# Kernel optimization log

Measured on AMD Instinct MI355X. Metric: run time of the kernel, lower is better.

Reference implementation:

```python
import jax, jax.numpy as jnp
import numpy as np


def setup_inputs() -> dict:
    key = jax.random.key(0)
    ks = jax.random.split(key, 7)
    B, I, H = 8192, 1024, 1024
    x = jax.random.normal(ks[0], (B, I), dtype=jnp.float32)
    h_prev = jax.random.normal(ks[1], (B, H), dtype=jnp.float32)
    C_prev = jax.random.normal(ks[2], (B, H), dtype=jnp.float32)
    W_f = jax.random.normal(ks[3], (I + H, H), dtype=jnp.float32) * 0.01
    W_i = jax.random.normal(ks[4], (I + H, H), dtype=jnp.float32) * 0.01
    W_C = jax.random.normal(ks[5], (I + H, H), dtype=jnp.float32) * 0.01
    W_o = jax.random.normal(ks[6], (I + H, H), dtype=jnp.float32) * 0.01
    b = jnp.zeros((H,), dtype=jnp.float32)
    return {"x": x, "h_prev": h_prev, "C_prev": C_prev,
            "W_f": W_f, "b_f": b, "W_i": W_i, "b_i": b,
            "W_C": W_C, "b_C": b, "W_o": W_o, "b_o": b}


def reference(x, h_prev, C_prev, W_f, b_f, W_i, b_i, W_C, b_C, W_o, b_o):
    combined = jnp.concatenate([x, h_prev], axis=1)  # [B, I+H]
    # Fuse the four gate GEMMs into one [B, I+H] x [I+H, 4H] matmul.
    W = jnp.concatenate([W_f, W_i, W_o, W_C], axis=1)  # [I+H, 4H]
    b = jnp.concatenate([b_f, b_i, b_o, b_C], axis=0)  # [4H]
    gates = combined @ W + b                            # [B, 4H]
    H = C_prev.shape[1]
    f_t = jax.nn.sigmoid(gates[:, 0:H])
    i_t = jax.nn.sigmoid(gates[:, H:2 * H])
    o_t = jax.nn.sigmoid(gates[:, 2 * H:3 * H])
    C_tilda = jnp.tanh(gates[:, 3 * H:4 * H])
    C_t = f_t * C_prev + i_t * C_tilda
    h_t = o_t * jnp.tanh(C_t)
    return (h_t, C_t)
```

## Files before the change

kernel.cpp:

```cpp
#include <hip/hip_runtime.h>
#include <hip/hip_bf16.h>

#define B_SZ 8192
#define IH   2048
#define H_SZ 1024
#define BM   256
#define BK   64
#define NT   (IH / BK)
#define NI   (NT / 2)
#define DBUF 65536
#define WOFF 32768

typedef __attribute__((ext_vector_type(8))) short  short8;
typedef __attribute__((ext_vector_type(4))) float  floatx4;

static __device__ __forceinline__ ushort f2bf(float f) {
  union { float f; unsigned u; } v; v.f = f;
  unsigned u = v.u;
  u += 0x7fffu + ((u >> 16) & 1u);
  return (ushort)(u >> 16);
}
static __device__ __forceinline__ float sigmoidf_(float x) {
  return 1.0f / (1.0f + __expf(-x));
}
static __device__ __forceinline__ float tanhf_(float x) {
  float ax = fabsf(x);
  float e = __expf(-2.0f * ax);
  float t = (1.0f - e) / (1.0f + e);
  return copysignf(t, x);
}
static __device__ __forceinline__ void gload_lds16(const void* gsrc, void* ldst) {
  __builtin_amdgcn_global_load_lds(
      (__attribute__((address_space(1))) const void*)gsrc,
      (__attribute__((address_space(3))) void*)ldst, 16, 0, 0);
}

__global__ __launch_bounds__(256) void convert_w_kernel(
    const float* __restrict__ Wf, const float* __restrict__ Wi,
    const float* __restrict__ Wo, const float* __restrict__ Wc,
    ushort* __restrict__ Wt) {
  __shared__ float tile[64][65];
  const int g  = blockIdx.z;
  const float* W = (g == 0) ? Wf : (g == 1) ? Wi : (g == 2) ? Wo : Wc;
  const int n0 = blockIdx.x * 64;
  const int k0 = blockIdx.y * 64;
  const int tid = threadIdx.x;
#pragma unroll
  for (int i = 0; i < 4; ++i) {
    int c = i * 256 + tid;
    int r = c >> 4, c4 = c & 15;
    float4 v = *(const float4*)(W + (size_t)(k0 + r) * H_SZ + n0 + c4 * 4);
    tile[r][c4 * 4 + 0] = v.x;
    tile[r][c4 * 4 + 1] = v.y;
    tile[r][c4 * 4 + 2] = v.z;
    tile[r][c4 * 4 + 3] = v.w;
  }
  __syncthreads();
  const int n  = tid >> 2;
  const int kc = (tid & 3) * 16;
  ushort o[16] __attribute__((aligned(16)));
#pragma unroll
  for (int e = 0; e < 16; ++e) o[e] = f2bf(tile[kc + e][n]);
  ushort* dst = Wt + ((size_t)g * H_SZ + n0 + n) * IH + k0 + kc;
  *(uint4*)(dst)     = *(uint4*)&o[0];
  *(uint4*)(dst + 8) = *(uint4*)&o[8];
}

__global__ __launch_bounds__(256) void convert_a_kernel(
    const float* __restrict__ x, const float* __restrict__ hp,
    ushort* __restrict__ Abf) {
  size_t idx = ((size_t)blockIdx.x * 256 + threadIdx.x) * 8;
  size_t row = idx >> 11;
  size_t col = idx & 2047;
  const float* src = (col < 1024) ? (x  + row * 1024 + col)
                                  : (hp + row * 1024 + (col - 1024));
  float4 v0 = *(const float4*)(src);
  float4 v1 = *(const float4*)(src + 4);
  ushort o[8] __attribute__((aligned(16)));
  o[0] = f2bf(v0.x); o[1] = f2bf(v0.y); o[2] = f2bf(v0.z); o[3] = f2bf(v0.w);
  o[4] = f2bf(v1.x); o[5] = f2bf(v1.y); o[6] = f2bf(v1.z); o[7] = f2bf(v1.w);
  *(uint4*)(Abf + idx) = *(uint4*)&o[0];
}

__global__ __launch_bounds__(512, 2) void lstm_fused_kernel(
    const float* __restrict__ Cp, const ushort* __restrict__ Wt,
    const ushort* __restrict__ Abf,
    const float* __restrict__ bf_, const float* __restrict__ bi_,
    const float* __restrict__ bo_, const float* __restrict__ bc_,
    float* __restrict__ out) {
  __shared__ char lds[2 * DBUF];

  const int bid = blockIdx.x;
  const int wg  = (bid & 7) * 64 + (bid >> 3);
  const int b0  = (wg >> 4) * BM;
  const int n0g = (wg & 15) * 64;

  const int tid = threadIdx.x;
  const int ln  = tid & 63;
  const int wv  = tid >> 6;
  const int wm  = wv >> 1, wn = wv & 1;

  floatx4 acc[4][8];
#pragma unroll
  for (int m = 0; m < 4; ++m)
#pragma unroll
    for (int j = 0; j < 8; ++j) acc[m][j] = {0.f, 0.f, 0.f, 0.f};

  const int sw  = (ln & 7) << 4;
  const int kb0 = (((ln >> 4) << 4)) ^ sw;
  const int kb1 = (64 + ((ln >> 4) << 4)) ^ sw;
  const int aR  = (wm * 64 + (ln & 15)) * 128;
  const int bR  = WOFF + (wn * 32 + (ln & 15)) * 128;
  int aB0[2], aB1[2], bB0[2], bB1[2];
#pragma unroll
  for (int d = 0; d < 2; ++d) {
    aB0[d] = d * DBUF + aR + kb0;  aB1[d] = d * DBUF + aR + kb1;
    bB0[d] = d * DBUF + bR + kb0;  bB1[d] = d * DBUF + bR + kb1;
  }

  const unsigned kcsw = ((tid & 7) * 16) ^ (((tid >> 3) & 7) << 4);
  const char*  AbfB = (const char*)Abf;
  const char*  WtB  = (const char*)Wt;
  unsigned aoff[2];
#pragma unroll
  for (int i = 0; i < 2; ++i)
    aoff[i] = ((unsigned)(b0 + i * 64 + (tid >> 3)) << 12) + kcsw;
  unsigned woff[2][2];
#pragma unroll
  for (int h = 0; h < 2; ++h)
#pragma unroll
    for (int i = 0; i < 2; ++i) {
      int nrt  = h * 128 + i * 64 + (tid >> 3);
      int g    = nrt >> 6, nloc = nrt & 63;
      woff[h][i] = ((unsigned)(g * H_SZ + n0g + nloc) << 12) + kcsw;
    }
  int dsto[2];
#pragma unroll
  for (int i = 0; i < 2; ++i) dsto[i] = (i * 512 + wv * 64) * 16;

#define STAGE_A(db, ktb, h)                                                   \
  do {                                                                        \
    gload_lds16(AbfB + (aoff[0] + ((unsigned)(h) << 19) + (unsigned)(ktb)),   \
                lds + (db) + (h) * 16384 + dsto[0]);                          \
    gload_lds16(AbfB + (aoff[1] + ((unsigned)(h) << 19) + (unsigned)(ktb)),   \
                lds + (db) + (h) * 16384 + dsto[1]);                          \
  } while (0)
#define STAGE_W(db, ktb, h)                                                   \
  do {                                                                        \
    gload_lds16(WtB + (woff[h][0] + (unsigned)(ktb)),                         \
                lds + (db) + WOFF + (h) * 16384 + dsto[0]);                   \
    gload_lds16(WtB + (woff[h][1] + (unsigned)(ktb)),                         \
                lds + (db) + WOFF + (h) * 16384 + dsto[1]);                   \
  } while (0)

  short8 aF[4][2];
  short8 bF[8][2];
#define RD_A(dbi, mf)                                                         \
  do {                                                                        \
    aF[mf][0] = *(const short8*)(lds + aB0[dbi] + (mf) * 2048);               \
    aF[mf][1] = *(const short8*)(lds + aB1[dbi] + (mf) * 2048);               \
  } while (0)
#define RD_B(dbi, j)                                                          \
  do {                                                                        \
    bF[j][0] = *(const short8*)(lds + bB0[dbi] + ((j) >> 1) * 8192 +          \
                                ((j) & 1) * 2048);                            \
    bF[j][1] = *(const short8*)(lds + bB1[dbi] + ((j) >> 1) * 8192 +          \
                                ((j) & 1) * 2048);                            \
  } while (0)
#define RDQA(d)  do { RD_A(d, 0); RD_A(d, 1); RD_A(d, 2); RD_A(d, 3); } while (0)
#define RDB03(d) do { RD_B(d, 0); RD_B(d, 1); RD_B(d, 2); RD_B(d, 3); } while (0)
#define RDB47(d) do { RD_B(d, 4); RD_B(d, 5); RD_B(d, 6); RD_B(d, 7); } while (0)
#define MFQ(jh)                                                               \
  do {                                                                        \
    __builtin_amdgcn_s_setprio(1);                                            \
    _Pragma("unroll")                                                         \
    for (int k_ = 0; k_ < 2; ++k_)                                            \
      _Pragma("unroll")                                                       \
      for (int mf_ = 0; mf_ < 4; ++mf_)                                       \
        _Pragma("unroll")                                                     \
        for (int j_ = 4 * (jh); j_ < 4 * (jh) + 4; ++j_)                      \
          acc[mf_][j_] = __builtin_amdgcn_mfma_f32_16x16x32_bf16(             \
              aF[mf_][k_], bF[j_][k_], acc[mf_][j_], 0, 0, 0);                \
    __builtin_amdgcn_s_setprio(0);                                            \
  } while (0)
#define BAR   __builtin_amdgcn_s_barrier()
#define VMC(n) asm volatile("s_waitcnt vmcnt(" #n ")" ::: "memory")

  STAGE_W(0, 0, 0); STAGE_A(0, 0, 0); STAGE_A(0, 0, 1); STAGE_W(0, 0, 1);
  STAGE_W(DBUF, 128, 0); STAGE_A(DBUF, 128, 0); STAGE_A(DBUF, 128, 1);
  VMC(6);
  BAR;

#pragma unroll 1
  for (int it = 0; it < NI; ++it) {
    const int kt1b  = (2 * it + 1) * 128;
    const int ktn0b = ((2 * it + 2) & 31) * 128;
    const int ktn1b = ((2 * it + 3) & 31) * 128;
    RDQA(0); RDB03(0);
    STAGE_W(DBUF, kt1b, 1);
    BAR; MFQ(0); BAR;
    RDB47(0);
    STAGE_W(0, ktn0b, 0); STAGE_A(0, ktn0b, 0);
    BAR; MFQ(1); VMC(4); BAR;
    RDQA(1); RDB03(1);
    STAGE_A(0, ktn0b, 1); STAGE_W(0, ktn0b, 1);
    BAR; MFQ(0); BAR;
    RDB47(1);
    STAGE_W(DBUF, ktn1b, 0); STAGE_A(DBUF, ktn1b, 0); STAGE_A(DBUF, ktn1b, 1);
    BAR; MFQ(1); VMC(6); BAR;
  }

  const int colq = ln & 15;
  const int rq   = ln >> 4;
  float* outh = out;
  float* outC = out + (size_t)B_SZ * H_SZ;
#pragma unroll
  for (int mf = 0; mf < 4; ++mf) {
#pragma unroll
    for (int ns = 0; ns < 2; ++ns) {
      int n = n0g + wn * 32 + ns * 16 + colq;
      float vbf = bf_[n], vbi = bi_[n], vbo = bo_[n], vbc = bc_[n];
#pragma unroll
      for (int r = 0; r < 4; ++r) {
        int row = b0 + wm * 64 + mf * 16 + rq * 4 + r;
        float fg = sigmoidf_(acc[mf][0 + ns][r] + vbf);
        float ig = sigmoidf_(acc[mf][2 + ns][r] + vbi);
        float og = sigmoidf_(acc[mf][4 + ns][r] + vbo);
        float cg = tanhf_  (acc[mf][6 + ns][r] + vbc);
        float cp = Cp[(size_t)row * H_SZ + n];
        float Ct = fg * cp + ig * cg;
        float ht = og * tanhf_(Ct);
        outh[(size_t)row * H_SZ + n] = ht;
        outC[(size_t)row * H_SZ + n] = Ct;
      }
    }
  }
#undef STAGE_A
#undef STAGE_W
#undef RD_A
#undef RD_B
#undef RDQA
#undef RDB03
#undef RDB47
#undef MFQ
#undef BAR
#undef VMC
}

extern "C" void kernel_launch(void* const* d_in, const int* in_sizes, int n_in,
                              void* d_out, int out_size, void* d_ws, size_t ws_size,
                              hipStream_t stream) {
  const float* x  = (const float*)d_in[0];
  const float* hp = (const float*)d_in[1];
  const float* Cp = (const float*)d_in[2];
  const float* Wf = (const float*)d_in[3];
  const float* bf = (const float*)d_in[4];
  const float* Wi = (const float*)d_in[5];
  const float* bi = (const float*)d_in[6];
  const float* Wc = (const float*)d_in[7];
  const float* bc = (const float*)d_in[8];
  const float* Wo = (const float*)d_in[9];
  const float* bo = (const float*)d_in[10];

  ushort* Wt  = (ushort*)d_ws;
  ushort* Abf = (ushort*)((char*)d_ws + (16u << 20));

  dim3 gridT(16, 32, 4);
  convert_w_kernel<<<gridT, 256, 0, stream>>>(Wf, Wi, Wo, Wc, Wt);
  convert_a_kernel<<<8192, 256, 0, stream>>>(x, hp, Abf);

  lstm_fused_kernel<<<512, 512, 0, stream>>>(Cp, Wt, Abf,
                                             bf, bi, bo, bc, (float*)d_out);
}
```

Baseline: 157.8 us.

## Load A fragments directly from global into registers, stage only W in LDS

The A (activation) tile is no longer staged through LDS. Each wave now loads its MFMA A fragments straight from global memory into registers, double-buffered across K steps. Only the W tile goes through LDS, which halves LDS use to 64KB and simplifies the pipeline to one barrier per K tile. The cost is that A rows are no longer shared through LDS between the two waves per row that both need them, so global/L2 traffic for A doubles. Register pressure also rises from the extra A buffers, and global latency is hidden only by one-tile prefetch with a full vmcnt(0) wait each tile.

```diff
diff --git a/kernel.cpp b/kernel.cpp
--- a/kernel.cpp
+++ b/kernel.cpp
@@ -7,9 +7,7 @@
 #define BM   256
 #define BK   64
 #define NT   (IH / BK)
-#define NI   (NT / 2)
-#define DBUF 65536
-#define WOFF 32768
+#define WBUF 32768
 
 typedef __attribute__((ext_vector_type(8))) short  short8;
 typedef __attribute__((ext_vector_type(4))) float  floatx4;
@@ -88,7 +86,7 @@
     const float* __restrict__ bf_, const float* __restrict__ bi_,
     const float* __restrict__ bo_, const float* __restrict__ bc_,
     float* __restrict__ out) {
-  __shared__ char lds[2 * DBUF];
+  __shared__ char lds[2 * WBUF];
 
   const int bid = blockIdx.x;
   const int wg  = (bid & 7) * 64 + (bid >> 3);
@@ -109,22 +107,23 @@
   const int sw  = (ln & 7) << 4;
   const int kb0 = (((ln >> 4) << 4)) ^ sw;
   const int kb1 = (64 + ((ln >> 4) << 4)) ^ sw;
-  const int aR  = (wm * 64 + (ln & 15)) * 128;
-  const int bR  = WOFF + (wn * 32 + (ln & 15)) * 128;
-  int aB0[2], aB1[2], bB0[2], bB1[2];
+  const int bR  = (wn * 32 + (ln & 15)) * 128;
+  int bB0[2], bB1[2];
 #pragma unroll
   for (int d = 0; d < 2; ++d) {
-    aB0[d] = d * DBUF + aR + kb0;  aB1[d] = d * DBUF + aR + kb1;
-    bB0[d] = d * DBUF + bR + kb0;  bB1[d] = d * DBUF + bR + kb1;
-  }
+    bB0[d] = d * WBUF + bR + kb0;
+    bB1[d] = d * WBUF + bR + kb1;
+  }
+
+  const char* aA[4];
+#pragma unroll
+  for (int mf = 0; mf < 4; ++mf)
+    aA[mf] = (const char*)Abf +
+             ((size_t)(b0 + wm * 64 + mf * 16 + (ln & 15)) << 12) +
+             ((ln >> 4) << 4);
 
   const unsigned kcsw = ((tid & 7) * 16) ^ (((tid >> 3) & 7) << 4);
-  const char*  AbfB = (const char*)Abf;
-  const char*  WtB  = (const char*)Wt;
-  unsigned aoff[2];
-#pragma unroll
-  for (int i = 0; i < 2; ++i)
-    aoff[i] = ((unsigned)(b0 + i * 64 + (tid >> 3)) << 12) + kcsw;
+  const char* WtB = (const char*)Wt;
   unsigned woff[2][2];
 #pragma unroll
   for (int h = 0; h < 2; ++h)
@@ -138,28 +137,16 @@
 #pragma unroll
   for (int i = 0; i < 2; ++i) dsto[i] = (i * 512 + wv * 64) * 16;
 
-#define STAGE_A(db, ktb, h)                                                   \
-  do {                                                                        \
-    gload_lds16(AbfB + (aoff[0] + ((unsigned)(h) << 19) + (unsigned)(ktb)),   \
+#define STAGE_W(db, ktb, h)                                                   \
+  do {                                                                        \
+    gload_lds16(WtB + (woff[h][0] + (unsigned)(ktb)),                         \
                 lds + (db) + (h) * 16384 + dsto[0]);                          \
-    gload_lds16(AbfB + (aoff[1] + ((unsigned)(h) << 19) + (unsigned)(ktb)),   \
+    gload_lds16(WtB + (woff[h][1] + (unsigned)(ktb)),                         \
                 lds + (db) + (h) * 16384 + dsto[1]);                          \
   } while (0)
-#define STAGE_W(db, ktb, h)                                                   \
-  do {                                                                        \
-    gload_lds16(WtB + (woff[h][0] + (unsigned)(ktb)),                         \
-                lds + (db) + WOFF + (h) * 16384 + dsto[0]);                   \
-    gload_lds16(WtB + (woff[h][1] + (unsigned)(ktb)),                         \
-                lds + (db) + WOFF + (h) * 16384 + dsto[1]);                   \
-  } while (0)
-
-  short8 aF[4][2];
+
+  short8 aCe[4][2], aCo[4][2];
   short8 bF[8][2];
-#define RD_A(dbi, mf)                                                         \
-  do {                                                                        \
-    aF[mf][0] = *(const short8*)(lds + aB0[dbi] + (mf) * 2048);               \
-    aF[mf][1] = *(const short8*)(lds + aB1[dbi] + (mf) * 2048);               \
-  } while (0)
 #define RD_B(dbi, j)                                                          \
   do {                                                                        \
     bF[j][0] = *(const short8*)(lds + bB0[dbi] + ((j) >> 1) * 8192 +          \
@@ -167,10 +154,9 @@
     bF[j][1] = *(const short8*)(lds + bB1[dbi] + ((j) >> 1) * 8192 +          \
                                 ((j) & 1) * 2048);                            \
   } while (0)
-#define RDQA(d)  do { RD_A(d, 0); RD_A(d, 1); RD_A(d, 2); RD_A(d, 3); } while (0)
 #define RDB03(d) do { RD_B(d, 0); RD_B(d, 1); RD_B(d, 2); RD_B(d, 3); } while (0)
 #define RDB47(d) do { RD_B(d, 4); RD_B(d, 5); RD_B(d, 6); RD_B(d, 7); } while (0)
-#define MFQ(jh)                                                               \
+#define MFQ(AC, jh)                                                           \
   do {                                                                        \
     __builtin_amdgcn_s_setprio(1);                                            \
     _Pragma("unroll")                                                         \
@@ -180,34 +166,41 @@
         _Pragma("unroll")                                                     \
         for (int j_ = 4 * (jh); j_ < 4 * (jh) + 4; ++j_)                      \
           acc[mf_][j_] = __builtin_amdgcn_mfma_f32_16x16x32_bf16(             \
-              aF[mf_][k_], bF[j_][k_], acc[mf_][j_], 0, 0, 0);                \
+              AC[mf_][k_], bF[j_][k_], acc[mf_][j_], 0, 0, 0);                \
     __builtin_amdgcn_s_setprio(0);                                            \
   } while (0)
 #define BAR   __builtin_amdgcn_s_barrier()
 #define VMC(n) asm volatile("s_waitcnt vmcnt(" #n ")" ::: "memory")
 
-  STAGE_W(0, 0, 0); STAGE_A(0, 0, 0); STAGE_A(0, 0, 1); STAGE_W(0, 0, 1);
-  STAGE_W(DBUF, 128, 0); STAGE_A(DBUF, 128, 0); STAGE_A(DBUF, 128, 1);
-  VMC(6);
+#define LOADA(AN, ktnb_)                                                      \
+  do {                                                                        \
+    _Pragma("unroll")                                                         \
+    for (int mf_ = 0; mf_ < 4; ++mf_) {                                       \
+      AN[mf_][0] = *(const short8*)(aA[mf_] + (ktnb_));                       \
+      AN[mf_][1] = *(const short8*)(aA[mf_] + (ktnb_) + 64);                  \
+    }                                                                         \
+  } while (0)
+
+#define TILE(BUFI, AC, AN, KTN)                                               \
+  do {                                                                        \
+    const int ktnb_ = ((KTN) & 31) * 128;                                     \
+    LOADA(AN, ktnb_);                                                         \
+    STAGE_W(((KTN) & 1) * WBUF, ktnb_, 0);                                    \
+    STAGE_W(((KTN) & 1) * WBUF, ktnb_, 1);                                    \
+    RDB03(BUFI); MFQ(AC, 0);                                                  \
+    RDB47(BUFI); MFQ(AC, 1);                                                  \
+    VMC(0); BAR;                                                              \
+  } while (0)
+
+  STAGE_W(0, 0, 0); STAGE_W(0, 0, 1);
+  LOADA(aCe, 0);
+  VMC(8);
   BAR;
 
 #pragma unroll 1
-  for (int it = 0; it < NI; ++it) {
-    const int kt1b  = (2 * it + 1) * 128;
-    const int ktn0b = ((2 * it + 2) & 31) * 128;
-    const int ktn1b = ((2 * it + 3) & 31) * 128;
-    RDQA(0); RDB03(0);
-    STAGE_W(DBUF, kt1b, 1);
-    BAR; MFQ(0); BAR;
-    RDB47(0);
-    STAGE_W(0, ktn0b, 0); STAGE_A(0, ktn0b, 0);
-    BAR; MFQ(1); VMC(4); BAR;
-    RDQA(1); RDB03(1);
-    STAGE_A(0, ktn0b, 1); STAGE_W(0, ktn0b, 1);
-    BAR; MFQ(0); BAR;
-    RDB47(1);
-    STAGE_W(DBUF, ktn1b, 0); STAGE_A(DBUF, ktn1b, 0); STAGE_A(DBUF, ktn1b, 1);
-    BAR; MFQ(1); VMC(6); BAR;
+  for (int it = 0; it < NT / 2; ++it) {
+    TILE(0, aCe, aCo, 2 * it + 1);
+    TILE(1, aCo, aCe, 2 * it + 2);
   }
 
   const int colq = ln & 15;
@@ -235,16 +228,15 @@
       }
     }
   }
-#undef STAGE_A
 #undef STAGE_W
-#undef RD_A
 #undef RD_B
-#undef RDQA
 #undef RDB03
 #undef RDB47
 #undef MFQ
 #undef BAR
 #undef VMC
+#undef LOADA
+#undef TILE
 }
 
 extern "C" void kernel_launch(void* const* d_in, const int* in_sizes, int n_in,
```

New measurement: 221.1 us. 40.1% more time.

## Remap waves to 2x4 grid with 128x16 warp tiles and finer LDS-read/MFMA interleave

Applied to the files above, without the earlier changes.

Changes the wave layout from 4x2 (64 rows x 32 cols per wave) to 2x4 (128 rows x 16 cols per wave), so each wave reads 8 A fragments and 4 B fragments instead of 4 and 8. The main loop is split into four smaller phases per K tile, each followed by an explicit lgkmcnt(0) wait and a scheduling barrier before its MFMA quarter. This is meant to rebalance LDS read traffic and overlap LDS reads with MFMA more finely. In exchange it adds more barriers per iteration and changes register pressure.

```diff
diff --git a/kernel.cpp b/kernel.cpp
--- a/kernel.cpp
+++ b/kernel.cpp
@@ -98,19 +98,20 @@
   const int tid = threadIdx.x;
   const int ln  = tid & 63;
   const int wv  = tid >> 6;
-  const int wm  = wv >> 1, wn = wv & 1;
-
-  floatx4 acc[4][8];
-#pragma unroll
-  for (int m = 0; m < 4; ++m)
-#pragma unroll
-    for (int j = 0; j < 8; ++j) acc[m][j] = {0.f, 0.f, 0.f, 0.f};
+  const int wm  = wv >> 2;
+  const int wn  = wv & 3;
+
+  floatx4 acc[8][4];
+#pragma unroll
+  for (int m = 0; m < 8; ++m)
+#pragma unroll
+    for (int j = 0; j < 4; ++j) acc[m][j] = {0.f, 0.f, 0.f, 0.f};
 
   const int sw  = (ln & 7) << 4;
   const int kb0 = (((ln >> 4) << 4)) ^ sw;
   const int kb1 = (64 + ((ln >> 4) << 4)) ^ sw;
-  const int aR  = (wm * 64 + (ln & 15)) * 128;
-  const int bR  = WOFF + (wn * 32 + (ln & 15)) * 128;
+  const int aR  = (wm * 128 + (ln & 15)) * 128;
+  const int bR  = WOFF + (wn * 16 + (ln & 15)) * 128;
   int aB0[2], aB1[2], bB0[2], bB1[2];
 #pragma unroll
   for (int d = 0; d < 2; ++d) {
@@ -153,8 +154,8 @@
                 lds + (db) + WOFF + (h) * 16384 + dsto[1]);                   \
   } while (0)
 
-  short8 aF[4][2];
-  short8 bF[8][2];
+  short8 aF[8][2];
+  short8 bF[4][2];
 #define RD_A(dbi, mf)                                                         \
   do {                                                                        \
     aF[mf][0] = *(const short8*)(lds + aB0[dbi] + (mf) * 2048);               \
@@ -162,33 +163,33 @@
   } while (0)
 #define RD_B(dbi, j)                                                          \
   do {                                                                        \
-    bF[j][0] = *(const short8*)(lds + bB0[dbi] + ((j) >> 1) * 8192 +          \
-                                ((j) & 1) * 2048);                            \
-    bF[j][1] = *(const short8*)(lds + bB1[dbi] + ((j) >> 1) * 8192 +          \
-                                ((j) & 1) * 2048);                            \
-  } while (0)
-#define RDQA(d)  do { RD_A(d, 0); RD_A(d, 1); RD_A(d, 2); RD_A(d, 3); } while (0)
-#define RDB03(d) do { RD_B(d, 0); RD_B(d, 1); RD_B(d, 2); RD_B(d, 3); } while (0)
-#define RDB47(d) do { RD_B(d, 4); RD_B(d, 5); RD_B(d, 6); RD_B(d, 7); } while (0)
-#define MFQ(jh)                                                               \
+    bF[j][0] = *(const short8*)(lds + bB0[dbi] + (j) * 8192);                 \
+    bF[j][1] = *(const short8*)(lds + bB1[dbi] + (j) * 8192);                 \
+  } while (0)
+#define MFQ(mh, jh)                                                           \
   do {                                                                        \
     __builtin_amdgcn_s_setprio(1);                                            \
     _Pragma("unroll")                                                         \
     for (int k_ = 0; k_ < 2; ++k_)                                            \
       _Pragma("unroll")                                                       \
-      for (int mf_ = 0; mf_ < 4; ++mf_)                                       \
+      for (int mf_ = 4 * (mh); mf_ < 4 * (mh) + 4; ++mf_)                     \
         _Pragma("unroll")                                                     \
-        for (int j_ = 4 * (jh); j_ < 4 * (jh) + 4; ++j_)                      \
+        for (int j_ = 2 * (jh); j_ < 2 * (jh) + 2; ++j_)                      \
           acc[mf_][j_] = __builtin_amdgcn_mfma_f32_16x16x32_bf16(             \
               aF[mf_][k_], bF[j_][k_], acc[mf_][j_], 0, 0, 0);                \
     __builtin_amdgcn_s_setprio(0);                                            \
   } while (0)
 #define BAR   __builtin_amdgcn_s_barrier()
-#define VMC(n) asm volatile("s_waitcnt vmcnt(" #n ")" ::: "memory")
+#define LGKM0                                                                 \
+  do {                                                                        \
+    asm volatile("s_waitcnt lgkmcnt(0)" ::: "memory");                        \
+    __builtin_amdgcn_sched_barrier(0);                                        \
+  } while (0)
+#define VMC6  asm volatile("s_waitcnt vmcnt(6)" ::: "memory")
 
   STAGE_W(0, 0, 0); STAGE_A(0, 0, 0); STAGE_A(0, 0, 1); STAGE_W(0, 0, 1);
   STAGE_W(DBUF, 128, 0); STAGE_A(DBUF, 128, 0); STAGE_A(DBUF, 128, 1);
-  VMC(6);
+  VMC6;
   BAR;
 
 #pragma unroll 1
@@ -196,55 +197,64 @@
     const int kt1b  = (2 * it + 1) * 128;
     const int ktn0b = ((2 * it + 2) & 31) * 128;
     const int ktn1b = ((2 * it + 3) & 31) * 128;
-    RDQA(0); RDB03(0);
+    RD_A(0, 0); RD_A(0, 1); RD_A(0, 2); RD_A(0, 3);
+    RD_B(0, 0); RD_B(0, 1);
     STAGE_W(DBUF, kt1b, 1);
-    BAR; MFQ(0); BAR;
-    RDB47(0);
-    STAGE_W(0, ktn0b, 0); STAGE_A(0, ktn0b, 0);
-    BAR; MFQ(1); VMC(4); BAR;
-    RDQA(1); RDB03(1);
-    STAGE_A(0, ktn0b, 1); STAGE_W(0, ktn0b, 1);
-    BAR; MFQ(0); BAR;
-    RDB47(1);
-    STAGE_W(DBUF, ktn1b, 0); STAGE_A(DBUF, ktn1b, 0); STAGE_A(DBUF, ktn1b, 1);
-    BAR; MFQ(1); VMC(6); BAR;
+    BAR; LGKM0; MFQ(0, 0); BAR;
+    RD_A(0, 4); RD_A(0, 5); RD_A(0, 6); RD_A(0, 7);
+    STAGE_W(0, ktn0b, 0);
+    BAR; LGKM0; MFQ(1, 0); BAR;
+    RD_B(0, 2); RD_B(0, 3);
+    STAGE_A(0, ktn0b, 0);
+    BAR; LGKM0; MFQ(0, 1); BAR;
+    STAGE_A(0, ktn0b, 1);
+    BAR; LGKM0; MFQ(1, 1);
+    VMC6; BAR;
+    RD_A(1, 0); RD_A(1, 1); RD_A(1, 2); RD_A(1, 3);
+    RD_B(1, 0); RD_B(1, 1);
+    STAGE_W(0, ktn0b, 1);
+    BAR; LGKM0; MFQ(0, 0); BAR;
+    RD_A(1, 4); RD_A(1, 5); RD_A(1, 6); RD_A(1, 7);
+    STAGE_W(DBUF, ktn1b, 0);
+    BAR; LGKM0; MFQ(1, 0); BAR;
+    RD_B(1, 2); RD_B(1, 3);
+    STAGE_A(DBUF, ktn1b, 0);
+    BAR; LGKM0; MFQ(0, 1); BAR;
+    STAGE_A(DBUF, ktn1b, 1);
+    BAR; LGKM0; MFQ(1, 1);
+    VMC6; BAR;
   }
 
   const int colq = ln & 15;
   const int rq   = ln >> 4;
   float* outh = out;
   float* outC = out + (size_t)B_SZ * H_SZ;
-#pragma unroll
-  for (int mf = 0; mf < 4; ++mf) {
-#pragma unroll
-    for (int ns = 0; ns < 2; ++ns) {
-      int n = n0g + wn * 32 + ns * 16 + colq;
-      float vbf = bf_[n], vbi = bi_[n], vbo = bo_[n], vbc = bc_[n];
-#pragma unroll
-      for (int r = 0; r < 4; ++r) {
-        int row = b0 + wm * 64 + mf * 16 + rq * 4 + r;
-        float fg = sigmoidf_(acc[mf][0 + ns][r] + vbf);
-        float ig = sigmoidf_(acc[mf][2 + ns][r] + vbi);
-        float og = sigmoidf_(acc[mf][4 + ns][r] + vbo);
-        float cg = tanhf_  (acc[mf][6 + ns][r] + vbc);
-        float cp = Cp[(size_t)row * H_SZ + n];
-        float Ct = fg * cp + ig * cg;
-        float ht = og * tanhf_(Ct);
-        outh[(size_t)row * H_SZ + n] = ht;
-        outC[(size_t)row * H_SZ + n] = Ct;
-      }
+  const int n = n0g + wn * 16 + colq;
+  const float vbf = bf_[n], vbi = bi_[n], vbo = bo_[n], vbc = bc_[n];
+#pragma unroll
+  for (int mf = 0; mf < 8; ++mf) {
+#pragma unroll
+    for (int r = 0; r < 4; ++r) {
+      int row = b0 + wm * 128 + mf * 16 + rq * 4 + r;
+      float fg = sigmoidf_(acc[mf][0][r] + vbf);
+      float ig = sigmoidf_(acc[mf][1][r] + vbi);
+      float og = sigmoidf_(acc[mf][2][r] + vbo);
+      float cg = tanhf_  (acc[mf][3][r] + vbc);
+      float cp = Cp[(size_t)row * H_SZ + n];
+      float Ct = fg * cp + ig * cg;
+      float ht = og * tanhf_(Ct);
+      outh[(size_t)row * H_SZ + n] = ht;
+      outC[(size_t)row * H_SZ + n] = Ct;
     }
   }
 #undef STAGE_A
 #undef STAGE_W
 #undef RD_A
 #undef RD_B
-#undef RDQA
-#undef RDB03
-#undef RDB47
 #undef MFQ
 #undef BAR
-#undef VMC
+#undef LGKM0
+#undef VMC6
 }
 
 extern "C" void kernel_launch(void* const* d_in, const int* in_sizes, int n_in,
```

Result: no change. 156.7 us (median of 2 runs) (-0.7%).
